# Kernel tuning notes

Measured on AMD Instinct MI355X. Metric: run time of the kernel, lower is better.

Reference implementation:

```python
import jax, jax.numpy as jnp
import numpy as np
from jax import lax

PI = jnp.pi
KX = jnp.array([[-1, 0, 1], [-2, 0, 2], [-1, 0, 1]], jnp.float32)
KY = jnp.array([[-1, -2, -1], [0, 0, 0], [1, 2, 1]], jnp.float32)
K45 = jnp.array([[-2, -1, 0], [-1, 0, 1], [0, 1, 2]], jnp.float32)
K135 = jnp.array([[0, 1, 2], [-1, 0, 1], [-2, -1, 0]], jnp.float32)


def _shift(x, dx, dy):
    # result[i, j] = x[clip(i - dx), clip(j - dy)]  (replicate boundary),
    # exactly matching the torch slice + replicate-pad neighbor construction.
    H, W = x.shape[2], x.shape[3]
    ri = jnp.clip(jnp.arange(H) - dx, 0, H - 1)
    ci = jnp.clip(jnp.arange(W) - dy, 0, W - 1)
    return x[:, :, ri[:, None], ci[None, :]]


def _adaptive_smoothing(f, k=10.0, iter_num=3):
    neighbors = [(-1, -1), (-1, 0), (-1, 1), (0, -1), (0, 0), (0, 1), (1, -1), (1, 0), (1, 1)]
    for _ in range(iter_num):
        Gx = (_shift(f, -1, 0) - _shift(f, 1, 0)) * 0.5   # gradient along H
        Gy = (_shift(f, 0, -1) - _shift(f, 0, 1)) * 0.5   # gradient along W
        w = jnp.exp(-(Gx * Gx + Gy * Gy) / (2.0 * k * k))
        f_new = jnp.zeros_like(f)
        w_sum = jnp.zeros_like(f)
        for dx, dy in neighbors:
            f_new = f_new + _shift(f, dx, dy) * _shift(w, dx, dy)
            w_sum = w_sum + _shift(w, dx, dy)
        f = f_new / jnp.maximum(w_sum, 1e-8)
    return f


def _dwconv(x, k2d):
    # depthwise 3x3 cross-correlation, zero padding (torch Conv2d semantics)
    C = x.shape[1]
    kern = jnp.broadcast_to(k2d[None, None], (C, 1, 3, 3)).astype(x.dtype)
    return lax.conv_general_dilated(x, kern, (1, 1), ((1, 1), (1, 1)),
                                    dimension_numbers=('NCHW', 'OIHW', 'NCHW'),
                                    feature_group_count=C)


def _sobel(x):
    return 0.5 * jnp.abs(_dwconv(x, KX)) + 0.5 * jnp.abs(_dwconv(x, KY))


def _hardswish(x):
    return x * jnp.clip(x + 3.0, 0.0, 6.0) / 6.0


def _canny(data, sigma, weight):
    blurred = _adaptive_smoothing(data, k=10.0, iter_num=3)
    sob = _sobel(blurred)
    B, C, H, W = sob.shape
    # torch.median: lower median = sorted[(n-1)//2]; .item() detaches it
    flat = jnp.sort(sob.reshape(B, C, H * W), axis=-1)
    med = lax.stop_gradient(jnp.mean(flat[:, :, (H * W - 1) // 2]))
    low = jnp.clip((1.0 - sigma) * med, 0.001, 1.0)
    high = jnp.clip((1.0 + sigma) * med, 0.001, 1.0)

    ex = _dwconv(blurred, KX)
    ey = _dwconv(blurred, KY)
    e45 = _dwconv(blurred, K45)
    e135 = _dwconv(blurred, K135)
    mag = jnp.sqrt(ex * ex + ey * ey + e45 * e45 + e135 * e135)
    ang = jnp.mod(jnp.arctan2(ey, ex), PI)

    dirs = jnp.array([0.0, PI / 4, PI / 2, 3 * PI / 4], jnp.float32)
    d = jnp.abs(ang[..., None] - dirs)
    dir_w = jax.nn.softmax(-jnp.minimum(d, PI - d) / 0.01, axis=-1)  # (B,C,H,W,4)

    pm = jnp.pad(mag, ((0, 0), (0, 0), (1, 1), (1, 1)), mode='edge')
    neigh = [(pm[:, :, 1:-1, :-2], pm[:, :, 1:-1, 2:]),
             (pm[:, :, :-2, :-2], pm[:, :, 2:, 2:]),
             (pm[:, :, :-2, 1:-1], pm[:, :, 2:, 1:-1]),
             (pm[:, :, :-2, 2:], pm[:, :, 2:, :-2])]
    sup = jnp.zeros_like(mag)
    for i, (n1, n2) in enumerate(neigh):  # fixed 4-direction loop
        sw = jax.nn.softmax(jnp.stack([mag, n1, n2], axis=-1) / 0.1, axis=-1)[..., 0]
        sup = sup + mag * sw * dir_w[..., i]

    mx = jnp.max(sup)
    sup = sup / jnp.where(mx > 0, mx, 1.0)

    Sh = _hardswish(sup - high)
    Sl = _hardswish(sup - low)
    ecanny = sup * (Sh + Sl)
    dilated = _dwconv(Sh, jnp.ones((3, 3), jnp.float32))
    result = ecanny + dilated * Sl * (1.0 - Sh)

    # enhance_edges with the ORIGINAL input
    result = (1.0 - weight) * result + weight * _sobel(data)
    rmin = jnp.min(result)
    rmax = jnp.max(result)
    return (result - rmin) / (rmax - rmin)


def setup_inputs() -> dict:
    key = jax.random.key(0)
    k1, k2 = jax.random.split(key)
    B, C, H, W = 8, 1, 512, 512
    return {
        'img1': jax.random.uniform(k1, (B, C, H, W), dtype=jnp.float32),
        'img2': jax.random.uniform(k2, (B, C, H, W), dtype=jnp.float32),
        'sigma1': jnp.float32(2.2),
        'enhance_weight1': jnp.float32(0.0),
        'sigma2': jnp.float32(2.2),
        'enhance_weight2': jnp.float32(0.0),
    }


def reference(img1, img2, sigma1, enhance_weight1, sigma2, enhance_weight2):
    s1 = 1.0 - jax.nn.sigmoid(sigma1)
    w1 = jax.nn.sigmoid(enhance_weight1)
    s2 = 1.0 - jax.nn.sigmoid(sigma2)
    w2 = jax.nn.sigmoid(enhance_weight2)
    m1 = _canny(img1, s1, w1)
    m2 = _canny(img2, s2, w2)
    f = (1.0 - m1) * (1.0 - m2) + m1 * m2
    return (1.0 - f, m1, m2)
```

## Files before the change

### kernel.cpp

```cpp
#include <hip/hip_runtime.h>

namespace {

constexpr int H = 512;
constexpr int W = 512;
constexpr int HW = H * W;
constexpr int PPS = 8;
constexpr int NP = 16;
constexpr int TX = 64;
constexpr int TY = 16;
constexpr int STY = 16;
constexpr int NBLK = (W / TX) * (H / TY) * NP;
constexpr int HBLK = NBLK / 2;
constexpr float PI_F = 3.14159265358979323846f;
constexpr int NBINS = 1024;
constexpr float BIN_SCALE = 512.0f;

__device__ __forceinline__ float hsw(float x) {
    float t = fminf(fmaxf(x + 3.0f, 0.0f), 6.0f);
    return x * t * (1.0f / 6.0f);
}

__device__ __forceinline__ const float* plane_ptr(const float* s1, const float* s2, int p) {
    return (p < PPS) ? (s1 + (size_t)p * HW) : (s2 + (size_t)(p - PPS) * HW);
}

__device__ __forceinline__ float wave_max(float v) {
    for (int o = 32; o > 0; o >>= 1) v = fmaxf(v, __shfl_down(v, o, 64));
    return v;
}
__device__ __forceinline__ float wave_min(float v) {
    for (int o = 32; o > 0; o >>= 1) v = fminf(v, __shfl_down(v, o, 64));
    return v;
}

__device__ __forceinline__ float atan_poly(float t) {
    float z = t * t;
    float p = -0.01172120f;
    p = p * z + 0.05265332f;
    p = p * z - 0.11643287f;
    p = p * z + 0.19354346f;
    p = p * z - 0.33262347f;
    p = p * z + 0.99997726f;
    return t * p;
}

__device__ __forceinline__ float sel4(int idx, float v0, float v1, float v2, float v3) {
    float a = (idx & 1) ? v1 : v0;
    float b = (idx & 1) ? v3 : v2;
    return (idx & 2) ? b : a;
}

__global__ void K_smooth(const float* __restrict__ s1, const float* __restrict__ s2,
                         float* __restrict__ fout, unsigned* __restrict__ hist) {
    int tid = threadIdx.y * 64 + threadIdx.x;
    if (hist) {
        int bid = (blockIdx.z * gridDim.y + blockIdx.y) * gridDim.x + blockIdx.x;
        if (bid < (NP * NBINS) / 256) hist[bid * 256 + tid] = 0;
    }
    int p = blockIdx.z;
    const float* f = plane_ptr(s1, s2, p);
    int j0 = blockIdx.x * 64, i0 = blockIdx.y * STY;
    __shared__ float fs[STY + 4][72];
    __shared__ float ws[STY + 2][66];

    bool interior = (i0 >= 2) && (i0 + STY + 1 <= H - 1) && (j0 >= 4) && (j0 + 67 <= W - 1);

    if (interior) {
        const float* fb = f + (i0 - 2) * W + (j0 - 4);
        for (int e = tid; e < (STY + 4) * 18; e += 256) {
            int y = e / 18, x4 = e % 18;
            float4 v = *(const float4*)(fb + y * W + x4 * 4);
            *(float4*)&fs[y][x4 * 4] = v;
        }
        __syncthreads();
        for (int e = tid; e < (STY + 2) * 66; e += 256) {
            int y = e / 66, x = e % 66;
            float gx = 0.5f * (fs[y + 2][x + 3] - fs[y][x + 3]);
            float gy = 0.5f * (fs[y + 1][x + 4] - fs[y + 1][x + 2]);
            ws[y][x] = __expf(-(gx * gx + gy * gy) * (1.0f / 200.0f));
        }
    } else {
        for (int e = tid; e < (STY + 4) * 72; e += 256) {
            int y = e / 72, x = e % 72;
            int gi = min(max(i0 - 2 + y, 0), H - 1);
            int gj = min(max(j0 - 4 + x, 0), W - 1);
            fs[y][x] = f[gi * W + gj];
        }
        __syncthreads();
        for (int e = tid; e < (STY + 2) * 66; e += 256) {
            int y = e / 66, x = e % 66;
            int r = min(max(i0 - 1 + y, 0), H - 1);
            int c = min(max(j0 - 1 + x, 0), W - 1);
            int yr = r - (i0 - 2), xc = c - (j0 - 4);
            int ym = max(r - 1, 0) - (i0 - 2), yp = min(r + 1, H - 1) - (i0 - 2);
            int xm = max(c - 1, 0) - (j0 - 4), xp = min(c + 1, W - 1) - (j0 - 4);
            float gx = 0.5f * (fs[yp][xc] - fs[ym][xc]);
            float gy = 0.5f * (fs[yr][xp] - fs[yr][xm]);
            ws[y][x] = __expf(-(gx * gx + gy * gy) * (1.0f / 200.0f));
        }
    }
    __syncthreads();

    int yl = threadIdx.y * 4;
    int xl = threadIdx.x;
    float rn[6], rd[6];
#pragma unroll
    for (int k = 0; k < 6; k++) {
        float w0 = ws[yl + k][xl], w1 = ws[yl + k][xl + 1], w2 = ws[yl + k][xl + 2];
        float fA = fs[yl + k + 1][xl + 3], fB = fs[yl + k + 1][xl + 4], fC = fs[yl + k + 1][xl + 5];
        rn[k] = fA * w0 + fB * w1 + fC * w2;
        rd[k] = w0 + w1 + w2;
    }
    size_t base = (size_t)p * HW + (i0 + yl) * W + (j0 + xl);
#pragma unroll
    for (int k = 0; k < 4; k++) {
        fout[base + (size_t)k * W] =
            (rn[k] + rn[k + 1] + rn[k + 2]) / fmaxf(rd[k] + rd[k + 1] + rd[k + 2], 1e-8f);
    }
}

__global__ void K_dnms(const float* __restrict__ blur, float* __restrict__ sup,
                       unsigned* __restrict__ hist, float* __restrict__ pmax) {
    int p = blockIdx.z;
    const float* f = blur + (size_t)p * HW;
    int j0 = blockIdx.x * TX, i0 = blockIdx.y * TY;
    __shared__ float fs0[TY + 4][72];
    __shared__ float ms[TY + 2][TX + 2];
    __shared__ unsigned histS[2][NBINS];
    __shared__ float wred[4];
    int tid = threadIdx.y * 64 + threadIdx.x;
    int hsel = threadIdx.y >> 1;

    bool interior = (i0 >= 2) && (i0 + TY + 1 <= H - 1) && (j0 >= 4) && (j0 + 67 <= W - 1);

    for (int e = tid; e < 2 * NBINS; e += 256) histS[e >> 10][e & (NBINS - 1)] = 0;
    if (interior) {
        const float* fb = f + (i0 - 2) * W + (j0 - 4);
        for (int e = tid; e < (TY + 4) * 18; e += 256) {
            int y = e / 18, x4 = e % 18;
            float4 v = *(const float4*)(fb + y * W + x4 * 4);
            *(float4*)&fs0[y][x4 * 4] = v;
        }
    } else {
        for (int e = tid; e < (TY + 4) * 72; e += 256) {
            int y = e / 72, x = e % 72;
            int gi = i0 - 2 + y, gj = j0 - 4 + x;
            fs0[y][x] = (gi >= 0 && gi < H && gj >= 0 && gj < W) ? f[gi * W + gj] : 0.0f;
        }
    }
    __syncthreads();

    int xl = threadIdx.x;
    int yb = threadIdx.y * 4;

    float fv[6][3];
#pragma unroll
    for (int rr = 0; rr < 6; rr++)
#pragma unroll
        for (int cc = 0; cc < 3; cc++)
            fv[rr][cc] = fs0[yb + 1 + rr][xl + 3 + cc];

    float exk[4], eyk[4];
#pragma unroll
    for (int k = 0; k < 4; k++) {
        float xmm = fv[k][0], xm0 = fv[k][1], xmp = fv[k][2];
        float x0m = fv[k + 1][0], x0p = fv[k + 1][2];
        float xpm = fv[k + 2][0], xp0 = fv[k + 2][1], xpp = fv[k + 2][2];
        float ex = (xmp - xmm) + 2.0f * (x0p - x0m) + (xpp - xpm);
        float ey = (xpm + 2.0f * xp0 + xpp) - (xmm + 2.0f * xm0 + xmp);
        float e45 = -2.0f * xmm - xm0 - x0m + x0p + xp0 + 2.0f * xpp;
        float e135 = xm0 + 2.0f * xmp - x0m + x0p - 2.0f * xpm - xp0;
        ms[yb + 1 + k][xl + 1] = sqrtf(ex * ex + ey * ey + e45 * e45 + e135 * e135);
        exk[k] = ex;
        eyk[k] = ey;
    }

    if (tid < 2 * (TX + 2) + 2 * TY) {
        int y, x;
        if (tid < TX + 2) { y = 0; x = tid; }
        else if (tid < 2 * (TX + 2)) { y = TY + 1; x = tid - (TX + 2); }
        else if (tid < 2 * (TX + 2) + TY) { y = tid - 2 * (TX + 2) + 1; x = 0; }
        else { y = tid - (2 * (TX + 2) + TY) + 1; x = TX + 1; }
        int rr, cc;
        if (interior) { rr = y + 1; cc = x + 3; }
        else {
            int r = min(max(i0 - 1 + y, 0), H - 1);
            int c = min(max(j0 - 1 + x, 0), W - 1);
            rr = r - i0 + 2; cc = c - j0 + 4;
        }
        float xmm = fs0[rr - 1][cc - 1], xm0 = fs0[rr - 1][cc], xmp = fs0[rr - 1][cc + 1];
        float x0m = fs0[rr][cc - 1], x0p = fs0[rr][cc + 1];
        float xpm = fs0[rr + 1][cc - 1], xp0 = fs0[rr + 1][cc], xpp = fs0[rr + 1][cc + 1];
        float ex = (xmp - xmm) + 2.0f * (x0p - x0m) + (xpp - xpm);
        float ey = (xpm + 2.0f * xp0 + xpp) - (xmm + 2.0f * xm0 + xmp);
        float e45 = -2.0f * xmm - xm0 - x0m + x0p + xp0 + 2.0f * xpp;
        float e135 = xm0 + 2.0f * xmp - x0m + x0p - 2.0f * xpm - xp0;
        ms[y][x] = sqrtf(ex * ex + ey * ey + e45 * e45 + e135 * e135);
    }
    __syncthreads();

    float msr[6][3];
#pragma unroll
    for (int rr = 0; rr < 6; rr++)
#pragma unroll
        for (int cc = 0; cc < 3; cc++)
            msr[rr][cc] = ms[yb + rr][xl + cc];

    float bmax = 0.0f;
#pragma unroll
    for (int k = 0; k < 4; k++) {
        float ex = exk[k], ey = eyk[k];

        float ax = fabsf(ex), ay = fabsf(ey);
        float mn = fminf(ax, ay), mxv = fmaxf(ax, ay);
        float tq = (mxv > 0.0f) ? __fdividef(mn, mxv) : 0.0f;
        float pang = atan_poly(tq);
        if (ay > ax) pang = 1.57079632679f - pang;
        bool obtuse = ((__float_as_uint(ex) ^ __float_as_uint(ey)) & 0x80000000u) != 0u;
        float a = obtuse ? PI_F - pang : pang;

        float fa = a * 1.27323954474f;
        float nf = floorf(fa + 0.5f);
        float diff = a - nf * 0.78539816340f;
        float delta = fabsf(diff);
        int n = (int)nf & 3;
        int m = ((diff >= 0.0f) ? (int)nf + 1 : (int)nf - 1) & 3;
        float t = __expf(200.0f * delta - 78.5398163397f);
        float u = __fdividef(1.0f, 1.0f + t);

        float m0 = msr[k + 1][1];
        float n1a = msr[k + 1][0], n1b = msr[k][0], n1c = msr[k][1], n1d = msr[k][2];
        float n2a = msr[k + 1][2], n2b = msr[k + 2][2], n2c = msr[k + 2][1], n2d = msr[k + 2][0];
        float n1n = sel4(n, n1a, n1b, n1c, n1d);
        float n2n = sel4(n, n2a, n2b, n2c, n2d);
        float n1m = sel4(m, n1a, n1b, n1c, n1d);
        float n2m = sel4(m, n2a, n2b, n2c, n2d);

        float g1n = __expf((n1n - m0) * 10.0f);
        float g2n = __expf((n2n - m0) * 10.0f);
        float g1m = __expf((n1m - m0) * 10.0f);
        float g2m = __expf((n2m - m0) * 10.0f);
        float swn = __fdividef(1.0f, 1.0f + g1n + g2n);
        float swm = __fdividef(1.0f, 1.0f + g1m + g2m);
        float s = m0 * u * (swn + t * swm);

        sup[(size_t)p * HW + (i0 + yb + k) * W + (j0 + xl)] = s;
        bmax = fmaxf(bmax, s);

        float sv = 0.5f * (ax + ay);
        int bin = min((int)(sv * BIN_SCALE), NBINS - 1);
        atomicAdd(&histS[hsel][bin], 1u);
    }

    float wv = wave_max(bmax);
    if ((tid & 63) == 0) wred[tid >> 6] = wv;
    __syncthreads();
    if (tid == 0) {
        int bflat = (blockIdx.z * gridDim.y + blockIdx.y) * gridDim.x + blockIdx.x;
        pmax[bflat] = fmaxf(fmaxf(wred[0], wred[1]), fmaxf(wred[2], wred[3]));
    }
    for (int e = tid; e < NBINS; e += 256) {
        unsigned v = histS[0][e] + histS[1][e];
        if (v) atomicAdd(&hist[p * NBINS + e], v);
    }
}

__global__ void K_stats(const unsigned* __restrict__ hist, const float* __restrict__ pmax,
                        float* __restrict__ medv, float* __restrict__ mx) {
    int b = blockIdx.x;
    int t = threadIdx.x;
    if (b < NP) {
        __shared__ unsigned sums[256];
        const unsigned* hp = hist + b * NBINS;
        unsigned s = 0;
        for (int q = 0; q < NBINS / 256; q++) s += hp[t * (NBINS / 256) + q];
        sums[t] = s;
        __syncthreads();
        for (int off = 1; off < 256; off <<= 1) {
            unsigned v = (t >= off) ? sums[t - off] : 0u;
            __syncthreads();
            sums[t] += v;
            __syncthreads();
        }
        const int k = (HW - 1) / 2;
        unsigned base = (t == 0) ? 0u : sums[t - 1];
        if ((int)base <= k && k < (int)sums[t]) {
            int cum = (int)base;
            int bin = t * (NBINS / 256);
            for (int q = 0; q < NBINS / 256; q++) {
                int c = (int)hp[t * (NBINS / 256) + q];
                if (cum + c > k) { bin = t * (NBINS / 256) + q; break; }
                cum += c;
            }
            medv[b] = ((float)bin + 0.5f) * (1.0f / BIN_SCALE);
        }
    } else {
        __shared__ float red[256];
        int s = b - NP;
        const float* base = pmax + s * HBLK;
        float v = -1e30f;
        for (int i = t; i < HBLK; i += 256) v = fmaxf(v, base[i]);
        red[t] = v;
        __syncthreads();
        for (int sft = 128; sft > 0; sft >>= 1) {
            if (t < sft) red[t] = fmaxf(red[t], red[t + sft]);
            __syncthreads();
        }
        if (t == 0) mx[s] = red[0];
    }
}

__global__ void K_result(const float* __restrict__ sup, const float* __restrict__ im1,
                         const float* __restrict__ im2, const float* __restrict__ medv,
                         const float* __restrict__ sg1, const float* __restrict__ ew1,
                         const float* __restrict__ sg2, const float* __restrict__ ew2,
                         const float* __restrict__ mx, float* __restrict__ res,
                         float* __restrict__ prmax, float* __restrict__ prmin) {
    int p = blockIdx.z;
    int s = p >> 3;
    float med = 0.125f * (medv[s * PPS + 0] + medv[s * PPS + 1] + medv[s * PPS + 2] +
                          medv[s * PPS + 3] + medv[s * PPS + 4] + medv[s * PPS + 5] +
                          medv[s * PPS + 6] + medv[s * PPS + 7]);
    float sgin = (s == 0) ? sg1[0] : sg2[0];
    float ewin = (s == 0) ? ew1[0] : ew2[0];
    float sig = 1.0f - 1.0f / (1.0f + __expf(-sgin));
    float lo = fminf(fmaxf((1.0f - sig) * med, 0.001f), 1.0f);
    float hi = fminf(fmaxf((1.0f + sig) * med, 0.001f), 1.0f);
    float wg = 1.0f / (1.0f + __expf(-ewin));
    float m = mx[s];
    float inv = 1.0f / ((m > 0.0f) ? m : 1.0f);

    const float* sp = sup + (size_t)p * HW;
    const float* op = plane_ptr(im1, im2, p);
    int j0 = blockIdx.x * TX, i0 = blockIdx.y * TY;
    __shared__ float hs2[TY + 2][72];
    __shared__ float og[TY + 2][72];
    __shared__ float ssn[TY][TX];
    __shared__ float wredx[4], wredn[4];
    int tid = threadIdx.y * 64 + threadIdx.x;

    bool interior = (i0 >= 1) && (i0 + TY <= H - 1) && (j0 >= 4) && (j0 + 67 <= W - 1);

    if (interior) {
        const float* spb = sp + (i0 - 1) * W + (j0 - 4);
        const float* opb = op + (i0 - 1) * W + (j0 - 4);
        for (int e = tid; e < (TY + 2) * 18; e += 256) {
            int y = e / 18, x4 = e % 18;
            float4 a = *(const float4*)(spb + y * W + x4 * 4);
            float4 o = *(const float4*)(opb + y * W + x4 * 4);
            float sv0 = a.x * inv, sv1 = a.y * inv, sv2 = a.z * inv, sv3 = a.w * inv;
            float4 hv;
            hv.x = hsw(sv0 - hi); hv.y = hsw(sv1 - hi);
            hv.z = hsw(sv2 - hi); hv.w = hsw(sv3 - hi);
            *(float4*)&hs2[y][x4 * 4] = hv;
            *(float4*)&og[y][x4 * 4] = o;
            if (y >= 1 && y <= TY) {
                int c0 = x4 * 4;
                if (c0 + 0 >= 4 && c0 + 0 <= 67) ssn[y - 1][c0 - 4] = sv0;
                if (c0 + 1 >= 4 && c0 + 1 <= 67) ssn[y - 1][c0 - 3] = sv1;
                if (c0 + 2 >= 4 && c0 + 2 <= 67) ssn[y - 1][c0 - 2] = sv2;
                if (c0 + 3 >= 4 && c0 + 3 <= 67) ssn[y - 1][c0 - 1] = sv3;
            }
        }
    } else {
        for (int e = tid; e < (TY + 2) * 72; e += 256) {
            int y = e / 72, x = e % 72;
            int gi = i0 - 1 + y, gj = j0 - 4 + x;
            float h = 0.0f, o = 0.0f;
            if (gi >= 0 && gi < H && gj >= 0 && gj < W) {
                float sv = sp[gi * W + gj] * inv;
                h = hsw(sv - hi);
                o = op[gi * W + gj];
                if (y >= 1 && y <= TY && x >= 4 && x <= 67) ssn[y - 1][x - 4] = sv;
            }
            hs2[y][x] = h;
            og[y][x] = o;
        }
    }
    __syncthreads();

    int yl = threadIdx.y * 4;
    int xl = threadIdx.x;
    float hrow[6], ddr[6], ssr[6];
#pragma unroll
    for (int k = 0; k < 6; k++) {
        float a = hs2[yl + k][xl + 3], bq = hs2[yl + k][xl + 4], c = hs2[yl + k][xl + 5];
        hrow[k] = a + bq + c;
        float oa = og[yl + k][xl + 3], ob = og[yl + k][xl + 4], oc = og[yl + k][xl + 5];
        ddr[k] = oc - oa;
        ssr[k] = oa + 2.0f * ob + oc;
    }

    float bmx = -1e30f, bmn = 1e30f;
    size_t gbase = (size_t)p * HW + (i0 + yl) * W + (j0 + xl);
#pragma unroll
    for (int k = 0; k < 4; k++) {
        float sn = ssn[yl + k][xl];
        float Sh = hs2[yl + k + 1][xl + 4];
        float Sl = hsw(sn - lo);
        float dil = hrow[k] + hrow[k + 1] + hrow[k + 2];
        float pre = sn * (Sh + Sl) + dil * Sl * (1.0f - Sh);
        float sob = 0.5f * fabsf(ddr[k] + 2.0f * ddr[k + 1] + ddr[k + 2]) +
                    0.5f * fabsf(ssr[k + 2] - ssr[k]);
        float r = (1.0f - wg) * pre + wg * sob;
        res[gbase + (size_t)k * W] = r;
        bmx = fmaxf(bmx, r);
        bmn = fminf(bmn, r);
    }

    float vx = wave_max(bmx), vn = wave_min(bmn);
    if ((tid & 63) == 0) { wredx[tid >> 6] = vx; wredn[tid >> 6] = vn; }
    __syncthreads();
    if (tid == 0) {
        int bflat = (blockIdx.z * gridDim.y + blockIdx.y) * gridDim.x + blockIdx.x;
        prmax[bflat] = fmaxf(fmaxf(wredx[0], wredx[1]), fmaxf(wredx[2], wredx[3]));
        prmin[bflat] = fminf(fminf(wredn[0], wredn[1]), fminf(wredn[2], wredn[3]));
    }
}

__global__ void K_final(const float* __restrict__ res, const float* __restrict__ prmax,
                        const float* __restrict__ prmin, float* __restrict__ out) {
    int tid = threadIdx.y * 64 + threadIdx.x;

    float vx0 = -1e30f, vn0 = 1e30f, vx1 = -1e30f, vn1 = 1e30f;
    for (int i = tid; i < HBLK; i += 256) {
        vx0 = fmaxf(vx0, prmax[i]);
        vn0 = fminf(vn0, prmin[i]);
        vx1 = fmaxf(vx1, prmax[HBLK + i]);
        vn1 = fminf(vn1, prmin[HBLK + i]);
    }
    vx0 = wave_max(vx0); vn0 = wave_min(vn0);
    vx1 = wave_max(vx1); vn1 = wave_min(vn1);
    __shared__ float sx0[4], sn0[4], sx1[4], sn1[4];
    if ((tid & 63) == 0) {
        int w = tid >> 6;
        sx0[w] = vx0; sn0[w] = vn0; sx1[w] = vx1; sn1[w] = vn1;
    }
    __syncthreads();
    float mx1 = fmaxf(fmaxf(sx0[0], sx0[1]), fmaxf(sx0[2], sx0[3]));
    float mn1 = fminf(fminf(sn0[0], sn0[1]), fminf(sn0[2], sn0[3]));
    float mx2 = fmaxf(fmaxf(sx1[0], sx1[1]), fmaxf(sx1[2], sx1[3]));
    float mn2 = fminf(fminf(sn1[0], sn1[1]), fminf(sn1[2], sn1[3]));
    float is1 = 1.0f / (mx1 - mn1);
    float is2 = 1.0f / (mx2 - mn2);

    int col4 = blockIdx.x * 64 + threadIdx.x;
    int i0 = blockIdx.y * 16 + threadIdx.y * 4;
    int p = blockIdx.z;
    const float4* r1p = (const float4*)(res + (size_t)p * HW);
    const float4* r2p = (const float4*)(res + (size_t)(p + PPS) * HW);
    float4* outc = (float4*)(out) + (size_t)p * (HW / 4);
    float4* out1 = (float4*)(out) + (size_t)(PPS + p) * (HW / 4);
    float4* out2 = (float4*)(out) + (size_t)(2 * PPS + p) * (HW / 4);

#pragma unroll
    for (int k = 0; k < 4; k++) {
        int row = i0 + k;
        float4 a = r1p[row * (W / 4) + col4];
        float4 b = r2p[row * (W / 4) + col4];
        float4 m1v, m2v, mcv;
        m1v.x = (a.x - mn1) * is1; m1v.y = (a.y - mn1) * is1;
        m1v.z = (a.z - mn1) * is1; m1v.w = (a.w - mn1) * is1;
        m2v.x = (b.x - mn2) * is2; m2v.y = (b.y - mn2) * is2;
        m2v.z = (b.z - mn2) * is2; m2v.w = (b.w - mn2) * is2;
        mcv.x = m1v.x + m2v.x - 2.0f * m1v.x * m2v.x;
        mcv.y = m1v.y + m2v.y - 2.0f * m1v.y * m2v.y;
        mcv.z = m1v.z + m2v.z - 2.0f * m1v.z * m2v.z;
        mcv.w = m1v.w + m2v.w - 2.0f * m1v.w * m2v.w;
        outc[row * (W / 4) + col4] = mcv;
        out1[row * (W / 4) + col4] = m1v;
        out2[row * (W / 4) + col4] = m2v;
    }
}

}

extern "C" void kernel_launch(void* const* d_in, const int* in_sizes, int n_in,
                              void* d_out, int out_size, void* d_ws, size_t ws_size,
                              hipStream_t stream) {
    const float* img1 = (const float*)d_in[0];
    const float* img2 = (const float*)d_in[1];
    const float* sg1 = (const float*)d_in[2];
    const float* ew1 = (const float*)d_in[3];
    const float* sg2 = (const float*)d_in[4];
    const float* ew2 = (const float*)d_in[5];
    float* out = (float*)d_out;

    float* A = (float*)d_ws;
    float* B = A + (size_t)NP * HW;
    float* C = B + (size_t)NP * HW;
    unsigned* hist = (unsigned*)(C + (size_t)NP * HW);
    float* medv = (float*)(hist + NP * NBINS);
    float* mx = medv + NP;
    float* pmax = mx + 2;
    float* prmax = pmax + NBLK;
    float* prmin = prmax + NBLK;

    dim3 blk(64, 4, 1);
    dim3 grdT(W / TX, H / TY, NP);
    dim3 grdS(W / 64, H / STY, NP);
    dim3 grdF(W / 256, H / 16, PPS);
    dim3 mblk(256, 1, 1);

    K_smooth<<<grdS, blk, 0, stream>>>(img1, img2, A, hist);
    K_smooth<<<grdS, blk, 0, stream>>>(A, A + (size_t)PPS * HW, B, nullptr);
    K_smooth<<<grdS, blk, 0, stream>>>(B, B + (size_t)PPS * HW, A, nullptr);

    K_dnms<<<grdT, blk, 0, stream>>>(A, C, hist, pmax);

    K_stats<<<dim3(NP + 2), mblk, 0, stream>>>(hist, pmax, medv, mx);

    K_result<<<grdT, blk, 0, stream>>>(C, img1, img2, medv, sg1, ew1, sg2, ew2, mx,
                                       B, prmax, prmin);

    K_final<<<grdF, blk, 0, stream>>>(B, prmax, prmin, out);
}
```

Measured before the change: 109.2 us.

## Fold stats and min/max reductions into last-block epilogues via atomic counters

Removes the separate K_stats launch by having the last finishing K_dnms block, detected through an atomic ticket counter, compute the per-plane histogram medians and the global maxima. K_result likewise has its last block reduce the per-block min/max into two scalars, so each K_final block only loads those scalars instead of re-reducing all partials. The shared histogram goes from two copies to one. This saves a kernel launch and redundant reduction work, at the cost of a serial tail in one block, threadfence overhead, and more shared-memory atomic contention on the single histogram.

```diff
diff --git a/kernel.cpp b/kernel.cpp
--- a/kernel.cpp
+++ b/kernel.cpp
@@ -52,11 +52,13 @@
 }
 
 __global__ void K_smooth(const float* __restrict__ s1, const float* __restrict__ s2,
-                         float* __restrict__ fout, unsigned* __restrict__ hist) {
+                         float* __restrict__ fout, unsigned* __restrict__ hist,
+                         unsigned* __restrict__ ctr) {
     int tid = threadIdx.y * 64 + threadIdx.x;
     if (hist) {
         int bid = (blockIdx.z * gridDim.y + blockIdx.y) * gridDim.x + blockIdx.x;
         if (bid < (NP * NBINS) / 256) hist[bid * 256 + tid] = 0;
+        if (bid == 64 && tid < 2) ctr[tid] = 0;
     }
     int p = blockIdx.z;
     const float* f = plane_ptr(s1, s2, p);
@@ -121,20 +123,23 @@
 }
 
 __global__ void K_dnms(const float* __restrict__ blur, float* __restrict__ sup,
-                       unsigned* __restrict__ hist, float* __restrict__ pmax) {
+                       unsigned* __restrict__ hist, float* __restrict__ pmax,
+                       float* __restrict__ medv, float* __restrict__ mx,
+                       unsigned* __restrict__ ctr) {
     int p = blockIdx.z;
     const float* f = blur + (size_t)p * HW;
     int j0 = blockIdx.x * TX, i0 = blockIdx.y * TY;
     __shared__ float fs0[TY + 4][72];
     __shared__ float ms[TY + 2][TX + 2];
-    __shared__ unsigned histS[2][NBINS];
-    __shared__ float wred[4];
+    __shared__ unsigned histS[NBINS];
+    __shared__ float wred[4], wred2[4];
+    __shared__ unsigned part[16][16];
+    __shared__ unsigned lastFlag;
     int tid = threadIdx.y * 64 + threadIdx.x;
-    int hsel = threadIdx.y >> 1;
 
     bool interior = (i0 >= 2) && (i0 + TY + 1 <= H - 1) && (j0 >= 4) && (j0 + 67 <= W - 1);
 
-    for (int e = tid; e < 2 * NBINS; e += 256) histS[e >> 10][e & (NBINS - 1)] = 0;
+    for (int e = tid; e < NBINS; e += 256) histS[e] = 0;
     if (interior) {
         const float* fb = f + (i0 - 2) * W + (j0 - 4);
         for (int e = tid; e < (TY + 4) * 18; e += 256) {
@@ -250,64 +255,60 @@
 
         float sv = 0.5f * (ax + ay);
         int bin = min((int)(sv * BIN_SCALE), NBINS - 1);
-        atomicAdd(&histS[hsel][bin], 1u);
+        atomicAdd(&histS[bin], 1u);
     }
 
     float wv = wave_max(bmax);
     if ((tid & 63) == 0) wred[tid >> 6] = wv;
     __syncthreads();
+    int bflat = (blockIdx.z * gridDim.y + blockIdx.y) * gridDim.x + blockIdx.x;
+    if (tid == 0) pmax[bflat] = fmaxf(fmaxf(wred[0], wred[1]), fmaxf(wred[2], wred[3]));
+    for (int e = tid; e < NBINS; e += 256)
+        if (histS[e]) atomicAdd(&hist[p * NBINS + e], histS[e]);
+
+    __syncthreads();
     if (tid == 0) {
-        int bflat = (blockIdx.z * gridDim.y + blockIdx.y) * gridDim.x + blockIdx.x;
-        pmax[bflat] = fmaxf(fmaxf(wred[0], wred[1]), fmaxf(wred[2], wred[3]));
-    }
-    for (int e = tid; e < NBINS; e += 256) {
-        unsigned v = histS[0][e] + histS[1][e];
-        if (v) atomicAdd(&hist[p * NBINS + e], v);
-    }
-}
-
-__global__ void K_stats(const unsigned* __restrict__ hist, const float* __restrict__ pmax,
-                        float* __restrict__ medv, float* __restrict__ mx) {
-    int b = blockIdx.x;
-    int t = threadIdx.x;
-    if (b < NP) {
-        __shared__ unsigned sums[256];
-        const unsigned* hp = hist + b * NBINS;
+        __threadfence();
+        lastFlag = (atomicAdd(&ctr[0], 1u) == NBLK - 1) ? 1u : 0u;
+    }
+    __syncthreads();
+    if (lastFlag) {
+        __threadfence();
+        int q = tid >> 4, g = tid & 15;
+        const unsigned* hp = hist + q * NBINS;
         unsigned s = 0;
-        for (int q = 0; q < NBINS / 256; q++) s += hp[t * (NBINS / 256) + q];
-        sums[t] = s;
-        __syncthreads();
-        for (int off = 1; off < 256; off <<= 1) {
-            unsigned v = (t >= off) ? sums[t - off] : 0u;
-            __syncthreads();
-            sums[t] += v;
-            __syncthreads();
-        }
-        const int k = (HW - 1) / 2;
-        unsigned base = (t == 0) ? 0u : sums[t - 1];
-        if ((int)base <= k && k < (int)sums[t]) {
-            int cum = (int)base;
-            int bin = t * (NBINS / 256);
-            for (int q = 0; q < NBINS / 256; q++) {
-                int c = (int)hp[t * (NBINS / 256) + q];
-                if (cum + c > k) { bin = t * (NBINS / 256) + q; break; }
+        for (int j = 0; j < 64; j++) s += hp[g * 64 + j];
+        part[q][g] = s;
+        __syncthreads();
+        if (g == 0) {
+            const int k = (HW - 1) / 2;
+            int cum = 0, chunk = 15;
+            for (int j = 0; j < 16; j++) {
+                int c = (int)part[q][j];
+                if (cum + c > k) { chunk = j; break; }
                 cum += c;
             }
-            medv[b] = ((float)bin + 0.5f) * (1.0f / BIN_SCALE);
-        }
-    } else {
-        __shared__ float red[256];
-        int s = b - NP;
-        const float* base = pmax + s * HBLK;
-        float v = -1e30f;
-        for (int i = t; i < HBLK; i += 256) v = fmaxf(v, base[i]);
-        red[t] = v;
-        __syncthreads();
-        for (int sft = 128; sft > 0; sft >>= 1) {
-            if (t < sft) red[t] = fmaxf(red[t], red[t + sft]);
-            __syncthreads();
-        }
-        if (t == 0) mx[s] = red[0];
+            int bin = chunk * 64 + 63;
+            for (int j = 0; j < 64; j++) {
+                int c = (int)hp[chunk * 64 + j];
+                if (cum + c > k) { bin = chunk * 64 + j; break; }
+                cum += c;
+            }
+            medv[q] = ((float)bin + 0.5f) * (1.0f / BIN_SCALE);
+        }
+        float v0 = -1e30f, v1 = -1e30f;
+        for (int i = tid; i < HBLK; i += 256) {
+            v0 = fmaxf(v0, pmax[i]);
+            v1 = fmaxf(v1, pmax[HBLK + i]);
+        }
+        v0 = wave_max(v0);
+        v1 = wave_max(v1);
+        if ((tid & 63) == 0) { wred[tid >> 6] = v0; wred2[tid >> 6] = v1; }
+        __syncthreads();
+        if (tid == 0) {
+            mx[0] = fmaxf(fmaxf(wred[0], wred[1]), fmaxf(wred[2], wred[3]));
+            mx[1] = fmaxf(fmaxf(wred2[0], wred2[1]), fmaxf(wred2[2], wred2[3]));
+        }
     }
 }
 
@@ -316,7 +317,9 @@
                          const float* __restrict__ sg1, const float* __restrict__ ew1,
                          const float* __restrict__ sg2, const float* __restrict__ ew2,
                          const float* __restrict__ mx, float* __restrict__ res,
-                         float* __restrict__ prmax, float* __restrict__ prmin) {
+                         float* __restrict__ prmax, float* __restrict__ prmin,
+                         float* __restrict__ rmaxv, float* __restrict__ rminv,
+                         unsigned* __restrict__ ctr) {
     int p = blockIdx.z;
     int s = p >> 3;
     float med = 0.125f * (medv[s * PPS + 0] + medv[s * PPS + 1] + medv[s * PPS + 2] +
@@ -338,6 +341,7 @@
     __shared__ float og[TY + 2][72];
     __shared__ float ssn[TY][TX];
     __shared__ float wredx[4], wredn[4];
+    __shared__ unsigned lastFlag;
     int tid = threadIdx.y * 64 + threadIdx.x;
 
     bool interior = (i0 >= 1) && (i0 + TY <= H - 1) && (j0 >= 4) && (j0 + 67 <= W - 1);
@@ -412,36 +416,46 @@
     float vx = wave_max(bmx), vn = wave_min(bmn);
     if ((tid & 63) == 0) { wredx[tid >> 6] = vx; wredn[tid >> 6] = vn; }
     __syncthreads();
+    int bflat = (blockIdx.z * gridDim.y + blockIdx.y) * gridDim.x + blockIdx.x;
     if (tid == 0) {
-        int bflat = (blockIdx.z * gridDim.y + blockIdx.y) * gridDim.x + blockIdx.x;
         prmax[bflat] = fmaxf(fmaxf(wredx[0], wredx[1]), fmaxf(wredx[2], wredx[3]));
         prmin[bflat] = fminf(fminf(wredn[0], wredn[1]), fminf(wredn[2], wredn[3]));
-    }
-}
-
-__global__ void K_final(const float* __restrict__ res, const float* __restrict__ prmax,
-                        const float* __restrict__ prmin, float* __restrict__ out) {
-    int tid = threadIdx.y * 64 + threadIdx.x;
-
-    float vx0 = -1e30f, vn0 = 1e30f, vx1 = -1e30f, vn1 = 1e30f;
-    for (int i = tid; i < HBLK; i += 256) {
-        vx0 = fmaxf(vx0, prmax[i]);
-        vn0 = fminf(vn0, prmin[i]);
-        vx1 = fmaxf(vx1, prmax[HBLK + i]);
-        vn1 = fminf(vn1, prmin[HBLK + i]);
-    }
-    vx0 = wave_max(vx0); vn0 = wave_min(vn0);
-    vx1 = wave_max(vx1); vn1 = wave_min(vn1);
-    __shared__ float sx0[4], sn0[4], sx1[4], sn1[4];
-    if ((tid & 63) == 0) {
-        int w = tid >> 6;
-        sx0[w] = vx0; sn0[w] = vn0; sx1[w] = vx1; sn1[w] = vn1;
-    }
-    __syncthreads();
-    float mx1 = fmaxf(fmaxf(sx0[0], sx0[1]), fmaxf(sx0[2], sx0[3]));
-    float mn1 = fminf(fminf(sn0[0], sn0[1]), fminf(sn0[2], sn0[3]));
-    float mx2 = fmaxf(fmaxf(sx1[0], sx1[1]), fmaxf(sx1[2], sx1[3]));
-    float mn2 = fminf(fminf(sn1[0], sn1[1]), fminf(sn1[2], sn1[3]));
+        __threadfence();
+        lastFlag = (atomicAdd(&ctr[1], 1u) == NBLK - 1) ? 1u : 0u;
+    }
+    __syncthreads();
+    if (lastFlag) {
+        __threadfence();
+        float vx0 = -1e30f, vn0 = 1e30f, vx1 = -1e30f, vn1 = 1e30f;
+        for (int i = tid; i < HBLK; i += 256) {
+            vx0 = fmaxf(vx0, prmax[i]);
+            vn0 = fminf(vn0, prmin[i]);
+            vx1 = fmaxf(vx1, prmax[HBLK + i]);
+            vn1 = fminf(vn1, prmin[HBLK + i]);
+        }
+        vx0 = wave_max(vx0); vn0 = wave_min(vn0);
+        vx1 = wave_max(vx1); vn1 = wave_min(vn1);
+        __syncthreads();
+        if ((tid & 63) == 0) { wredx[tid >> 6] = vx0; wredn[tid >> 6] = vn0; }
+        __syncthreads();
+        if (tid == 0) {
+            rmaxv[0] = fmaxf(fmaxf(wredx[0], wredx[1]), fmaxf(wredx[2], wredx[3]));
+            rminv[0] = fminf(fminf(wredn[0], wredn[1]), fminf(wredn[2], wredn[3]));
+        }
+        __syncthreads();
+        if ((tid & 63) == 0) { wredx[tid >> 6] = vx1; wredn[tid >> 6] = vn1; }
+        __syncthreads();
+        if (tid == 0) {
+            rmaxv[1] = fmaxf(fmaxf(wredx[0], wredx[1]), fmaxf(wredx[2], wredx[3]));
+            rminv[1] = fminf(fminf(wredn[0], wredn[1]), fminf(wredn[2], wredn[3]));
+        }
+    }
+}
+
+__global__ void K_final(const float* __restrict__ res, const float* __restrict__ rmaxv,
+                        const float* __restrict__ rminv, float* __restrict__ out) {
+    float mx1 = rmaxv[0], mn1 = rminv[0];
+    float mx2 = rmaxv[1], mn2 = rminv[1];
     float is1 = 1.0f / (mx1 - mn1);
     float is2 = 1.0f / (mx2 - mn2);
 
@@ -493,7 +507,10 @@
     unsigned* hist = (unsigned*)(C + (size_t)NP * HW);
     float* medv = (float*)(hist + NP * NBINS);
     float* mx = medv + NP;
-    float* pmax = mx + 2;
+    float* rmaxv = mx + 2;
+    float* rminv = rmaxv + 2;
+    unsigned* ctr = (unsigned*)(rminv + 2);
+    float* pmax = (float*)(ctr + 2);
     float* prmax = pmax + NBLK;
     float* prmin = prmax + NBLK;
 
@@ -501,18 +518,15 @@
     dim3 grdT(W / TX, H / TY, NP);
     dim3 grdS(W / 64, H / STY, NP);
     dim3 grdF(W / 256, H / 16, PPS);
-    dim3 mblk(256, 1, 1);
-
-    K_smooth<<<grdS, blk, 0, stream>>>(img1, img2, A, hist);
-    K_smooth<<<grdS, blk, 0, stream>>>(A, A + (size_t)PPS * HW, B, nullptr);
-    K_smooth<<<grdS, blk, 0, stream>>>(B, B + (size_t)PPS * HW, A, nullptr);
-
-    K_dnms<<<grdT, blk, 0, stream>>>(A, C, hist, pmax);
-
-    K_stats<<<dim3(NP + 2), mblk, 0, stream>>>(hist, pmax, medv, mx);
+
+    K_smooth<<<grdS, blk, 0, stream>>>(img1, img2, A, hist, ctr);
+    K_smooth<<<grdS, blk, 0, stream>>>(A, A + (size_t)PPS * HW, B, nullptr, nullptr);
+    K_smooth<<<grdS, blk, 0, stream>>>(B, B + (size_t)PPS * HW, A, nullptr, nullptr);
+
+    K_dnms<<<grdT, blk, 0, stream>>>(A, C, hist, pmax, medv, mx, ctr);
 
     K_result<<<grdT, blk, 0, stream>>>(C, img1, img2, medv, sg1, ew1, sg2, ew2, mx,
-                                       B, prmax, prmin);
-
-    K_final<<<grdF, blk, 0, stream>>>(B, prmax, prmin, out);
-}
+                                       B, prmax, prmin, rmaxv, rminv, ctr);
+
+    K_final<<<grdF, blk, 0, stream>>>(B, rmaxv, rminv, out);
+}
```

Measured after the change: 322.9 us. 2.96x slower.
